# Performance work log

Measured on AMD Instinct MI355X. Metric: run time of the kernel, lower is better.

The kernel has to match this reference:

```python
import jax, jax.numpy as jnp
import numpy as np

# irreps layout: in/out = 32x0e + 8x1o  (dim 32 + 24 = 56), sh = 1x0e + 1x1o (dim 4)
NS, NV = 32, 8
N_NODES, N_EDGES, N_EDGE_FEAT, HIDDEN = 10000, 100000, 64, 64
W_NUMEL = NS*NS + NS*NV + NV*NV + NV*NS  # 1600
EPS = 1e-5
# path normalization (e3nn-style 'component'/'element'):
# fan_in into 0e output = 32 (0x0 path) + 8 (1x1 path) = 40; same for 1o output.
INV40 = 1.0 / np.sqrt(40.0)            # paths with trivial/identity CG net factor
INV120 = 1.0 / np.sqrt(120.0)          # paths with w3j = delta/sqrt(3) extra factor


def setup_inputs() -> dict:
    key = jax.random.key(0)
    ks = jax.random.split(key, 12)
    node_attr = jax.random.normal(ks[0], (N_NODES, 56), dtype=jnp.float32)
    edge_attr = jax.random.normal(ks[1], (N_EDGES, N_EDGE_FEAT), dtype=jnp.float32)
    edge_sh = jax.random.normal(ks[2], (N_EDGES, 4), dtype=jnp.float32)
    edge_index = jax.random.randint(ks[3], (2, N_EDGES), 0, N_NODES, dtype=jnp.int64)
    s1 = 1.0 / np.sqrt(N_EDGE_FEAT)
    s2 = 1.0 / np.sqrt(HIDDEN)
    fc1_w = jax.random.normal(ks[4], (N_EDGE_FEAT, HIDDEN), dtype=jnp.float32) * s1
    fc1_b = jnp.zeros((HIDDEN,), dtype=jnp.float32)
    fc2_w = jax.random.normal(ks[5], (HIDDEN, W_NUMEL), dtype=jnp.float32) * s2
    fc2_b = jnp.zeros((W_NUMEL,), dtype=jnp.float32)
    bn_gamma0 = jnp.ones((NS,), dtype=jnp.float32)
    bn_beta0 = jnp.zeros((NS,), dtype=jnp.float32)
    bn_gamma1 = jnp.ones((NV,), dtype=jnp.float32)
    return dict(node_attr=node_attr, edge_attr=edge_attr, edge_sh=edge_sh,
                edge_index=edge_index, fc1_w=fc1_w, fc1_b=fc1_b,
                fc2_w=fc2_w, fc2_b=fc2_b, bn_gamma0=bn_gamma0,
                bn_beta0=bn_beta0, bn_gamma1=bn_gamma1)


def _forward(node_attr, edge_attr, edge_sh, fc1_w, fc1_b, fc2_w, fc2_b,
             bn_gamma0, bn_beta0, bn_gamma1, edge_index):
    E = edge_attr.shape[0]
    N = node_attr.shape[0]
    edge_src, edge_dst = edge_index[0], edge_index[1]

    # edge MLP -> per-edge tensor-product weights [E, 1600]
    h = jax.nn.relu(edge_attr @ fc1_w + fc1_b)
    w = h @ fc2_w + fc2_b
    o1 = NS * NS            # 0e x 0e -> 0e
    o2 = o1 + NS * NV       # 0e x 1o -> 1o
    o3 = o2 + NV * NV       # 1o x 0e -> 1o
    w00 = w[:, :o1].reshape(E, NS, NS)
    w01 = w[:, o1:o2].reshape(E, NS, NV)
    w10 = w[:, o2:o3].reshape(E, NV, NV)
    w11 = w[:, o3:].reshape(E, NV, NS)

    # gather node features at destination, split into scalar / vector irreps
    x = node_attr[edge_dst]                  # [E, 56]
    x0 = x[:, :NS]                           # [E, 32] scalars
    x1 = x[:, NS:].reshape(E, NV, 3)         # [E, 8, 3] l=1 vectors
    s0 = edge_sh[:, 0]                       # [E]
    s1 = edge_sh[:, 1:4]                     # [E, 3]

    # Clebsch-Gordan paths (w3j(1,1,0)=w3j(1,0,1)=w3j(0,1,1)=delta/sqrt(3))
    out0 = jnp.einsum('eu,euw->ew', x0 * s0[:, None], w00) * INV40 \
         + jnp.einsum('eui,ei,euw->ew', x1, s1, w11) * INV120
    out1 = jnp.einsum('eu,ei,euw->ewi', x0, s1, w01) * INV40 \
         + jnp.einsum('eui,euw->ewi', x1 * s0[:, None, None], w10) * INV40
    tp_out = jnp.concatenate([out0, out1.reshape(E, NV * 3)], axis=-1)  # [E, 56]

    # scatter-mean over edge_src
    sums = jax.ops.segment_sum(tp_out, edge_src, num_segments=N)
    cnt = jax.ops.segment_sum(jnp.ones((E,), tp_out.dtype), edge_src, num_segments=N)
    out = sums / jnp.maximum(cnt, 1.0)[:, None]

    # residual (in_dim == out_dim, pad is a no-op)
    out = out + node_attr

    # e3nn-style BatchNorm (training statistics, reduce='mean')
    sc = out[:, :NS]
    vec = out[:, NS:].reshape(N, NV, 3)
    m = sc.mean(axis=0)
    sc_c = sc - m
    var = (sc_c ** 2).mean(axis=0)
    sc_n = sc_c * jax.lax.rsqrt(var + EPS) * bn_gamma0 + bn_beta0
    vnorm = (vec ** 2).mean(axis=-1).mean(axis=0)          # [NV]
    vec_n = vec * (jax.lax.rsqrt(vnorm + EPS) * bn_gamma1)[None, :, None]
    return jnp.concatenate([sc_n, vec_n.reshape(N, NV * 3)], axis=-1)


def reference(node_attr, edge_attr, edge_sh, edge_index, fc1_w, fc1_b,
              fc2_w, fc2_b, bn_gamma0, bn_beta0, bn_gamma1):
    return _forward(node_attr, edge_attr, edge_sh, fc1_w, fc1_b, fc2_w,
                    fc2_b, bn_gamma0, bn_beta0, bn_gamma1, edge_index)
```

## Files before the change

### kernel.cpp

```cpp
#include <hip/hip_runtime.h>

typedef __attribute__((ext_vector_type(4)))  float f32x4;
typedef __attribute__((ext_vector_type(16))) float f32x16;
typedef __attribute__((ext_vector_type(8)))  short bf16x8;
typedef __attribute__((ext_vector_type(4)))  short short4v;

#define NEDGE 100000
#define NNODE 10000
#define INV40f 0.15811388300841897f
#define INV120f 0.09128709291752769f

__device__ inline short f2bf(float f) {
    unsigned u = __builtin_bit_cast(unsigned, f);
    u = (u + 0x7fffu + ((u >> 16) & 1u)) >> 16;
    return (short)u;
}

__device__ __forceinline__ float bperm(int byteIdx, float v) {
    return __builtin_bit_cast(float,
        __builtin_amdgcn_ds_bpermute(byteIdx, __builtin_bit_cast(int, v)));
}

__device__ __forceinline__ void stage16(const void* gsrc, void* ldst) {
    __builtin_amdgcn_global_load_lds(
        (const __attribute__((address_space(1))) unsigned*)gsrc,
        (__attribute__((address_space(3))) unsigned*)(unsigned long long)(uintptr_t)ldst,
        16, 0, 0);
}

#define MFMA32(A,B,C) __builtin_amdgcn_mfma_f32_32x32x16_bf16((A),(B),(C),0,0,0)

__global__ __launch_bounds__(256) void prep(const float* __restrict__ fc1_w,
                                            const float* __restrict__ fc2_w,
                                            short* __restrict__ fc1_wt,
                                            short* __restrict__ fc2_wt,
                                            float* __restrict__ stats,
                                            int* __restrict__ hist) {
    const int b = blockIdx.x, t = threadIdx.x;
    if (b < 25) {
        __shared__ short tile[64 * 66];
        const int c0 = b * 64;
        #pragma unroll
        for (int rep = 0; rep < 16; rep++) {
            const int idx = rep * 256 + t;
            const int k = idx >> 6, c = idx & 63;
            tile[k * 66 + c] = f2bf(fc2_w[(size_t)k * 1600 + c0 + c]);
        }
        __syncthreads();
        #pragma unroll
        for (int rep = 0; rep < 16; rep++) {
            const int idx = rep * 256 + t;
            const int c = idx >> 6, k = idx & 63;
            fc2_wt[(size_t)(c0 + c) * 64 + k] = tile[k * 66 + c];
        }
    } else if (b == 25) {
        #pragma unroll
        for (int rep = 0; rep < 16; rep++) {
            const int i = rep * 256 + t;
            fc1_wt[(i & 63) * 64 + (i >> 6)] = f2bf(fc1_w[i]);
        }
    } else if (b == 26) {
        if (t < 72) stats[t] = 0.0f;
    } else {
        const int i = (b - 27) * 256 + t;
        if (i < NNODE) hist[i] = 0;
    }
}

__global__ __launch_bounds__(256, 2) void edge_fused(
    const float* __restrict__ node_attr,
    const float* __restrict__ edge_attr,
    const float* __restrict__ edge_sh,
    const int*   __restrict__ edge_index,
    const float* __restrict__ fc1_b,
    const float* __restrict__ fc2_b,
    const short* __restrict__ fc1_wt,
    const short* __restrict__ fc2_wt,
    float* __restrict__ tp_out,
    int*   __restrict__ hist)
{
    __shared__ __align__(16) char lds[41216];
    char* cbA = lds;
    char* cbB = lds + 16384;
    float* bias_s = (float*)(lds + 34816);

    const int tid  = threadIdx.x;
    const int wid  = tid >> 6;
    const int wtid = tid & 63;
    const int l31  = wtid & 31;
    const int half = wtid >> 5;
    const int e0   = blockIdx.x * 128 + wid * 32;
    const bool active = (e0 < NEDGE);

    char*  h_s = cbB + wid * 4096;
    float* shb = (float*)(lds + 32768 + wid * 512);
    const int swzl = (l31 & 7) << 4;

#define STAGE1(CH, BUF, J) do { \
        const int _o = (wid * 4 + (J)) * 1024 + wtid * 16; \
        const int _g = _o ^ (((_o >> 7) & 7) << 4); \
        stage16((const char*)fc2_wt + (CH) * 16384 + _g, (BUF) + (wid * 4 + (J)) * 1024); \
    } while (0)
#define STAGE_FULL(CH, BUF) do { STAGE1(CH,BUF,0); STAGE1(CH,BUF,1); STAGE1(CH,BUF,2); STAGE1(CH,BUF,3); } while (0)

    STAGE_FULL(0, cbA);

    *(f32x4*)(bias_s + tid * 4) = *(const f32x4*)(fc2_b + tid * 4);
    if (tid < 144)
        *(f32x4*)(bias_s + (tid + 256) * 4) = *(const f32x4*)(fc2_b + (tid + 256) * 4);

    int dst_r = 0;
    if (active && wtid < 32) {
        dst_r = edge_index[NEDGE + e0 + wtid];
        atomicAdd(&hist[edge_index[e0 + wtid]], 1);
        *(f32x4*)(shb + wtid * 4) = *(const f32x4*)(edge_sh + (size_t)(e0 + wtid) * 4);
    }

    bf16x8 hb[4];
    f32x4 shv = {0.f, 0.f, 0.f, 0.f};
    float cb1r[16], c10r[12], c11r[4];
    int vs[2];
    vs[0] = l31 * 4;
    vs[1] = (32 + l31) * 4;

    if (active) {
        const int dstm = __shfl(dst_r, l31, 64);
        const float* nap = node_attr + (size_t)dstm * 56;
        shv = *(const f32x4*)(shb + l31 * 4);

        const f32x4 t0 = *(const f32x4*)(nap + half * 16);
        const f32x4 t1 = *(const f32x4*)(nap + half * 16 + 4);
        const f32x4 t2 = *(const f32x4*)(nap + half * 16 + 8);
        const f32x4 t3 = *(const f32x4*)(nap + half * 16 + 12);
        #pragma unroll
        for (int j = 0; j < 4; j++) {
            cb1r[j]      = INV40f * t0[j];
            cb1r[4 + j]  = INV40f * t1[j];
            cb1r[8 + j]  = INV40f * t2[j];
            cb1r[12 + j] = INV40f * t3[j];
        }
        const f32x4 y0 = *(const f32x4*)(nap + 32 + half * 12);
        const f32x4 y1 = *(const f32x4*)(nap + 32 + half * 12 + 4);
        const f32x4 y2 = *(const f32x4*)(nap + 32 + half * 12 + 8);
        float xx[12];
        #pragma unroll
        for (int j = 0; j < 4; j++) { xx[j] = y0[j]; xx[4 + j] = y1[j]; xx[8 + j] = y2[j]; }
        const float i40s0 = INV40f * shv[0];
        #pragma unroll
        for (int k = 0; k < 12; k++) c10r[k] = i40s0 * xx[k];
        #pragma unroll
        for (int e = 0; e < 4; e++)
            c11r[e] = INV120f * (xx[e*3]*shv[1] + xx[e*3+1]*shv[2] + xx[e*3+2]*shv[3]);

        const float* pe = edge_attr + (size_t)(e0 + l31) * 64 + half * 8;
        bf16x8 eb[4];
        #pragma unroll
        for (int s = 0; s < 4; s++) {
            const f32x4 a = *(const f32x4*)(pe + s * 16);
            const f32x4 b = *(const f32x4*)(pe + s * 16 + 4);
            #pragma unroll
            for (int i = 0; i < 4; i++) { eb[s][i] = f2bf(a[i]); eb[s][4 + i] = f2bf(b[i]); }
        }
        #pragma unroll
        for (int g = 0; g < 2; g++) {
            f32x16 c;
            #pragma unroll
            for (int q = 0; q < 4; q++) {
                const f32x4 bq = *(const f32x4*)(fc1_b + g*32 + q*8 + half*4);
                c[q*4+0] = bq[0]; c[q*4+1] = bq[1]; c[q*4+2] = bq[2]; c[q*4+3] = bq[3];
            }
            #pragma unroll
            for (int s = 0; s < 4; s++) {
                const bf16x8 af = *(const bf16x8*)(fc1_wt + (g*32 + l31)*64 + s*16 + half*8);
                c = MFMA32(af, eb[s], c);
            }
            #pragma unroll
            for (int q = 0; q < 4; q++) {
                short4v p;
                #pragma unroll
                for (int j = 0; j < 4; j++) p[j] = f2bf(fmaxf(c[q*4+j], 0.0f));
                *(short4v*)(h_s + (l31*128 + ((g*64 + q*16 + half*8) ^ swzl)));
                *(short4v*)(h_s + (l31*128 + ((g*64 + q*16 + half*8) ^ swzl))) = p;
            }
        }
        #pragma unroll
        for (int s = 0; s < 4; s++)
            hb[s] = *(const bf16x8*)(h_s + (l31*128 + ((s*32 + half*16) ^ swzl)));
    }

    float acc0[16] = {};
    float ab1[4] = {0,0,0,0};
    float b2[12] = {};

    auto mload = [&](const char* cb, int go, int G) -> f32x16 {
        f32x16 c;
        #pragma unroll
        for (int q = 0; q < 4; q++) {
            const f32x4 bq = *(const f32x4*)(bias_s + G*32 + q*8 + half*4);
            c[q*4+0] = bq[0]; c[q*4+1] = bq[1]; c[q*4+2] = bq[2]; c[q*4+3] = bq[3];
        }
        #pragma unroll
        for (int s = 0; s < 4; s++) {
            const bf16x8 a = *(const bf16x8*)(cb + go*4096 + l31*128 + ((s*32 + half*16) ^ swzl));
            c = MFMA32(a, hb[s], c);
        }
        return c;
    };

    auto cons_w00 = [&](const char* cb, int ch) {
        #pragma unroll
        for (int go = 0; go < 4; go++) {
            const int G = ch * 4 + go;
            const f32x16 c = mload(cb, go, G);
            const float cv = shv[0] * bperm(vs[G >> 4], cb1r[G & 15]);
            #pragma unroll
            for (int r = 0; r < 16; r++) acc0[r] += cv * c[r];
        }
    };
    auto cons_w01 = [&](const char* cb, int Gl0) {
        #pragma unroll
        for (int go = 0; go < 4; go++) {
            const int Gl = Gl0 + go;
            const f32x16 c = mload(cb, go, 32 + Gl);
            #pragma unroll
            for (int q = 0; q < 4; q++) {
                const int u = Gl * 4 + q;
                const float cvq = bperm(vs[u >> 4], cb1r[u & 15]);
                #pragma unroll
                for (int j = 0; j < 4; j++) ab1[j] += cvq * c[q*4+j];
            }
        }
    };
    auto cons_w10 = [&](const char* cb) {
        #pragma unroll
        for (int go = 0; go < 2; go++) {
            const f32x16 c = mload(cb, go, 40 + go);
            #pragma unroll
            for (int q = 0; q < 4; q++) {
                const int u = go * 4 + q;
                #pragma unroll
                for (int i = 0; i < 3; i++) {
                    const float cv = bperm(vs[u >> 2], c10r[(u & 3) * 3 + i]);
                    #pragma unroll
                    for (int j = 0; j < 4; j++) b2[j*3+i] += cv * c[q*4+j];
                }
            }
        }
    };
    auto cons_w11_2 = [&](const char* cb, int goBase, int Gl0) {
        #pragma unroll
        for (int go = 0; go < 2; go++) {
            const int Gl = Gl0 + go;
            const f32x16 c = mload(cb, goBase + go, 42 + Gl);
            const float cv = bperm(vs[Gl >> 2], c11r[Gl & 3]);
            #pragma unroll
            for (int r = 0; r < 16; r++) acc0[r] += cv * c[r];
        }
    };
    auto cons_w11_4 = [&](const char* cb, int Gl0) {
        #pragma unroll
        for (int go = 0; go < 4; go++) {
            const int Gl = Gl0 + go;
            const f32x16 c = mload(cb, go, 42 + Gl);
            const float cv = bperm(vs[Gl >> 2], c11r[Gl & 3]);
            #pragma unroll
            for (int r = 0; r < 16; r++) acc0[r] += cv * c[r];
        }
    };

    __syncthreads();
    STAGE_FULL(1,  cbB); if (active) cons_w00(cbA, 0); __syncthreads();
    STAGE_FULL(2,  cbA); if (active) cons_w00(cbB, 1); __syncthreads();
    STAGE_FULL(3,  cbB); if (active) cons_w00(cbA, 2); __syncthreads();
    STAGE_FULL(4,  cbA); if (active) cons_w00(cbB, 3); __syncthreads();
    STAGE_FULL(5,  cbB); if (active) cons_w00(cbA, 4); __syncthreads();
    STAGE_FULL(6,  cbA); if (active) cons_w00(cbB, 5); __syncthreads();
    STAGE_FULL(7,  cbB); if (active) cons_w00(cbA, 6); __syncthreads();
    STAGE_FULL(8,  cbA); if (active) cons_w00(cbB, 7); __syncthreads();
    STAGE_FULL(9,  cbB); if (active) cons_w01(cbA, 0); __syncthreads();
    STAGE_FULL(10, cbA); if (active) cons_w01(cbB, 4); __syncthreads();
    STAGE_FULL(11, cbB); if (active) { cons_w10(cbA); cons_w11_2(cbA, 2, 0); } __syncthreads();
    STAGE_FULL(12, cbA); if (active) cons_w11_4(cbB, 2); __syncthreads();
                         if (active) cons_w11_2(cbA, 0, 6);

    if (!active) return;

    float* orow = tp_out + (size_t)(e0 + l31) * 56;
    #pragma unroll
    for (int q = 0; q < 4; q++)
        *(f32x4*)(orow + q*8 + half*4) = f32x4{acc0[q*4], acc0[q*4+1], acc0[q*4+2], acc0[q*4+3]};
    float ov[12];
    #pragma unroll
    for (int j = 0; j < 4; j++) {
        ov[j*3 + 0] = shv[1] * ab1[j] + b2[j*3 + 0];
        ov[j*3 + 1] = shv[2] * ab1[j] + b2[j*3 + 1];
        ov[j*3 + 2] = shv[3] * ab1[j] + b2[j*3 + 2];
    }
    float* p1 = orow + 32 + half * 12;
    *(f32x4*)(p1)     = f32x4{ov[0], ov[1], ov[2],  ov[3]};
    *(f32x4*)(p1 + 4) = f32x4{ov[4], ov[5], ov[6],  ov[7]};
    *(f32x4*)(p1 + 8) = f32x4{ov[8], ov[9], ov[10], ov[11]};
#undef STAGE1
#undef STAGE_FULL
}

__global__ __launch_bounds__(256) void scan_hist(const int* __restrict__ hist,
                                                 int* __restrict__ offsets,
                                                 int* __restrict__ cursor) {
    __shared__ int wsum[4];
    const int t = threadIdx.x;
    const int lane = t & 63;
    const int w = t >> 6;
    const int n0 = t * 40;
    int s = 0;
    if (n0 < NNODE) {
        for (int j = 0; j < 40; j++) s += hist[n0 + j];
    }
    int incl = s;
    #pragma unroll
    for (int d = 1; d < 64; d <<= 1) {
        const int v = __shfl_up(incl, d, 64);
        if (lane >= d) incl += v;
    }
    if (lane == 63) wsum[w] = incl;
    __syncthreads();
    int base = 0;
    for (int ww = 0; ww < 4; ww++) base += (ww < w) ? wsum[ww] : 0;
    if (n0 < NNODE) {
        int run = base + incl - s;
        for (int j = 0; j < 40; j++) {
            const int h = hist[n0 + j];
            offsets[n0 + j] = run; cursor[n0 + j] = run; run += h;
        }
    }
    if (t == 0) offsets[NNODE] = NEDGE;
}

__global__ __launch_bounds__(256) void fill_perm(const int* __restrict__ edge_index,
                                                 int* __restrict__ cursor,
                                                 int* __restrict__ perm) {
    const int e = blockIdx.x * 256 + threadIdx.x;
    if (e < NEDGE) {
        const int s = edge_index[e];
        const int p = atomicAdd(&cursor[s], 1);
        perm[p] = e;
    }
}

__global__ __launch_bounds__(256) void node_agg(
    const float* __restrict__ tp_out, const int* __restrict__ offsets,
    const int* __restrict__ perm,
    const float* __restrict__ node_attr, float* __restrict__ out,
    float* __restrict__ stats)
{
    __shared__ float part[72];
    const int tid = threadIdx.x;
    if (tid < 72) part[tid] = 0.0f;
    __syncthreads();
    const int n = blockIdx.x * 16 + (tid >> 4);
    const int q = tid & 15;
    if (n < NNODE && q < 14) {
        const int st = offsets[n], en = offsets[n + 1];
        f32x4 acc = {0.f, 0.f, 0.f, 0.f};
        for (int r = st; r < en; r++)
            acc += *(const f32x4*)(tp_out + (size_t)perm[r] * 56 + q * 4);
        const float inv = 1.0f / fmaxf((float)(en - st), 1.0f);
        const int c0 = q * 4;
        const f32x4 res = *(const f32x4*)(node_attr + (size_t)n * 56 + c0);
        f32x4 val;
        #pragma unroll
        for (int j = 0; j < 4; j++) {
            val[j] = acc[j] * inv + res[j];
            const int c = c0 + j;
            if (c < 32) {
                atomicAdd(&part[c], val[j]);
                atomicAdd(&part[32 + c], val[j] * val[j]);
            } else {
                atomicAdd(&part[64 + (c - 32) / 3], val[j] * val[j]);
            }
        }
        *(f32x4*)(out + (size_t)n * 56 + c0) = val;
    }
    __syncthreads();
    if (tid < 72) unsafeAtomicAdd(&stats[tid], part[tid]);
}

__global__ __launch_bounds__(256) void node_norm(
    float* __restrict__ out, const float* __restrict__ stats,
    const float* __restrict__ g0, const float* __restrict__ b0,
    const float* __restrict__ g1)
{
    const int id = blockIdx.x * 256 + threadIdx.x;
    if (id >= NNODE * 56) return;
    const int c = id % 56;
    float val = out[id];
    if (c < 32) {
        const float m   = stats[c]      * (1.0f / NNODE);
        const float ex2 = stats[32 + c] * (1.0f / NNODE);
        const float var = ex2 - m * m;
        val = (val - m) * rsqrtf(var + 1e-5f) * g0[c] + b0[c];
    } else {
        const int v = (c - 32) / 3;
        const float vn = stats[64 + v] * (1.0f / (3.0f * NNODE));
        val = val * rsqrtf(vn + 1e-5f) * g1[v];
    }
    out[id] = val;
}

extern "C" void kernel_launch(void* const* d_in, const int* in_sizes, int n_in,
                              void* d_out, int out_size, void* d_ws, size_t ws_size,
                              hipStream_t stream) {
    const float* node_attr = (const float*)d_in[0];
    const float* edge_attr = (const float*)d_in[1];
    const float* edge_sh   = (const float*)d_in[2];
    const int*   edge_index= (const int*)  d_in[3];
    const float* fc1_w     = (const float*)d_in[4];
    const float* fc1_b     = (const float*)d_in[5];
    const float* fc2_w     = (const float*)d_in[6];
    const float* fc2_b     = (const float*)d_in[7];
    const float* g0        = (const float*)d_in[8];
    const float* b0        = (const float*)d_in[9];
    const float* g1        = (const float*)d_in[10];
    float* out = (float*)d_out;

    char* ws = (char*)d_ws;
    float* stats   = (float*)(ws + 0);
    int*   hist    = (int*)  (ws + 288);
    int*   offsets = (int*)  (ws + 40288);
    int*   cursor  = (int*)  (ws + 80320);
    int*   perm    = (int*)  (ws + 120320);
    short* fc1_wt  = (short*)(ws + 520320);
    short* fc2_wt  = (short*)(ws + 528512);
    float* tp_out  = (float*)(ws + 733312);

    prep<<<67, 256, 0, stream>>>(fc1_w, fc2_w, fc1_wt, fc2_wt, stats, hist);
    edge_fused<<<782, 256, 0, stream>>>(node_attr, edge_attr, edge_sh, edge_index,
                                        fc1_b, fc2_b, fc1_wt, fc2_wt, tp_out, hist);
    scan_hist<<<1, 256, 0, stream>>>(hist, offsets, cursor);
    fill_perm<<<391, 256, 0, stream>>>(edge_index, cursor, perm);
    node_agg<<<625, 256, 0, stream>>>(tp_out, offsets, perm, node_attr, out, stats);
    node_norm<<<2188, 256, 0, stream>>>(out, stats, g0, b0, g1);
}
```

Measured before the change: 105.0 us.

## Triple-buffer fc2 weight staging with explicit vmcnt waits and raw barriers

```diff
diff --git a/kernel.cpp b/kernel.cpp
--- a/kernel.cpp
+++ b/kernel.cpp
@@ -79,10 +79,11 @@
     float* __restrict__ tp_out,
     int*   __restrict__ hist)
 {
-    __shared__ __align__(16) char lds[41216];
-    char* cbA = lds;
-    char* cbB = lds + 16384;
-    float* bias_s = (float*)(lds + 34816);
+    __shared__ __align__(16) char lds[57600];
+    char* bufs0 = lds;
+    char* bufs1 = lds + 16384;
+    char* bufs2 = lds + 32768;
+    float* bias_s = (float*)(lds + 51200);
 
     const int tid  = threadIdx.x;
     const int wid  = tid >> 6;
@@ -92,8 +93,8 @@
     const int e0   = blockIdx.x * 128 + wid * 32;
     const bool active = (e0 < NEDGE);
 
-    char*  h_s = cbB + wid * 4096;
-    float* shb = (float*)(lds + 32768 + wid * 512);
+    char*  h_s = bufs2 + wid * 4096;
+    float* shb = (float*)(lds + 49152 + wid * 512);
     const int swzl = (l31 & 7) << 4;
 
 #define STAGE1(CH, BUF, J) do { \
@@ -103,7 +104,6 @@
     } while (0)
 #define STAGE_FULL(CH, BUF) do { STAGE1(CH,BUF,0); STAGE1(CH,BUF,1); STAGE1(CH,BUF,2); STAGE1(CH,BUF,3); } while (0)
 
-    STAGE_FULL(0, cbA);
 
     *(f32x4*)(bias_s + tid * 4) = *(const f32x4*)(fc2_b + tid * 4);
     if (tid < 144)
@@ -179,7 +179,6 @@
                 short4v p;
                 #pragma unroll
                 for (int j = 0; j < 4; j++) p[j] = f2bf(fmaxf(c[q*4+j], 0.0f));
-                *(short4v*)(h_s + (l31*128 + ((g*64 + q*16 + half*8) ^ swzl)));
                 *(short4v*)(h_s + (l31*128 + ((g*64 + q*16 + half*8) ^ swzl))) = p;
             }
         }
@@ -187,6 +186,15 @@
         for (int s = 0; s < 4; s++)
             hb[s] = *(const bf16x8*)(h_s + (l31*128 + ((s*32 + half*16) ^ swzl)));
     }
+
+    asm volatile("s_waitcnt lgkmcnt(0)" ::: "memory");
+    __builtin_amdgcn_sched_barrier(0);
+    __builtin_amdgcn_s_barrier();
+    __builtin_amdgcn_sched_barrier(0);
+
+    STAGE_FULL(0, bufs0);
+    STAGE_FULL(1, bufs1);
+    STAGE_FULL(2, bufs2);
 
     float acc0[16] = {};
     float ab1[4] = {0,0,0,0};
@@ -268,20 +276,35 @@
         }
     };
 
-    __syncthreads();
-    STAGE_FULL(1,  cbB); if (active) cons_w00(cbA, 0); __syncthreads();
-    STAGE_FULL(2,  cbA); if (active) cons_w00(cbB, 1); __syncthreads();
-    STAGE_FULL(3,  cbB); if (active) cons_w00(cbA, 2); __syncthreads();
-    STAGE_FULL(4,  cbA); if (active) cons_w00(cbB, 3); __syncthreads();
-    STAGE_FULL(5,  cbB); if (active) cons_w00(cbA, 4); __syncthreads();
-    STAGE_FULL(6,  cbA); if (active) cons_w00(cbB, 5); __syncthreads();
-    STAGE_FULL(7,  cbB); if (active) cons_w00(cbA, 6); __syncthreads();
-    STAGE_FULL(8,  cbA); if (active) cons_w00(cbB, 7); __syncthreads();
-    STAGE_FULL(9,  cbB); if (active) cons_w01(cbA, 0); __syncthreads();
-    STAGE_FULL(10, cbA); if (active) cons_w01(cbB, 4); __syncthreads();
-    STAGE_FULL(11, cbB); if (active) { cons_w10(cbA); cons_w11_2(cbA, 2, 0); } __syncthreads();
-    STAGE_FULL(12, cbA); if (active) cons_w11_4(cbB, 2); __syncthreads();
-                         if (active) cons_w11_2(cbA, 0, 6);
+#define WAITBAR(N) do { \
+        asm volatile("s_waitcnt vmcnt(" N ")" ::: "memory"); \
+        __builtin_amdgcn_sched_barrier(0); \
+        __builtin_amdgcn_s_barrier(); \
+        __builtin_amdgcn_sched_barrier(0); \
+    } while (0)
+#define ENDPHASE() do { \
+        __builtin_amdgcn_s_barrier(); \
+        __builtin_amdgcn_sched_barrier(0); \
+    } while (0)
+
+    WAITBAR("8"); if (active) cons_w00(bufs0, 0); ENDPHASE(); STAGE_FULL(3,  bufs0);
+    WAITBAR("8"); if (active) cons_w00(bufs1, 1); ENDPHASE(); STAGE_FULL(4,  bufs1);
+    WAITBAR("8"); if (active) cons_w00(bufs2, 2); ENDPHASE(); STAGE_FULL(5,  bufs2);
+    WAITBAR("8"); if (active) cons_w00(bufs0, 3); ENDPHASE(); STAGE_FULL(6,  bufs0);
+    WAITBAR("8"); if (active) cons_w00(bufs1, 4); ENDPHASE(); STAGE_FULL(7,  bufs1);
+    WAITBAR("8"); if (active) cons_w00(bufs2, 5); ENDPHASE(); STAGE_FULL(8,  bufs2);
+    WAITBAR("8"); if (active) cons_w00(bufs0, 6); ENDPHASE(); STAGE_FULL(9,  bufs0);
+    WAITBAR("8"); if (active) cons_w00(bufs1, 7); ENDPHASE(); STAGE_FULL(10, bufs1);
+    WAITBAR("8"); if (active) cons_w01(bufs2, 0); ENDPHASE(); STAGE_FULL(11, bufs2);
+    WAITBAR("8"); if (active) cons_w01(bufs0, 4); ENDPHASE(); STAGE_FULL(12, bufs0);
+    WAITBAR("8"); if (active) { cons_w10(bufs1); cons_w11_2(bufs1, 2, 0); } ENDPHASE();
+    WAITBAR("4"); if (active) cons_w11_4(bufs2, 2); ENDPHASE();
+    WAITBAR("0"); if (active) cons_w11_2(bufs0, 0, 6);
+
+#undef WAITBAR
+#undef ENDPHASE
+#undef STAGE1
+#undef STAGE_FULL
 
     if (!active) return;
 
@@ -300,8 +323,6 @@
     *(f32x4*)(p1)     = f32x4{ov[0], ov[1], ov[2],  ov[3]};
     *(f32x4*)(p1 + 4) = f32x4{ov[4], ov[5], ov[6],  ov[7]};
     *(f32x4*)(p1 + 8) = f32x4{ov[8], ov[9], ov[10], ov[11]};
-#undef STAGE1
-#undef STAGE_FULL
 }
 
 __global__ __launch_bounds__(256) void scan_hist(const int* __restrict__ hist,
```

Measured after the change: 104.0 us. About the same (-1.0%).

## Pre-permute fc2 weights into MFMA fragment order and widen histogram scan

Applied to the files above, without the earlier changes.

```diff
diff --git a/kernel.cpp b/kernel.cpp
--- a/kernel.cpp
+++ b/kernel.cpp
@@ -47,11 +47,16 @@
             tile[k * 66 + c] = f2bf(fc2_w[(size_t)k * 1600 + c0 + c]);
         }
         __syncthreads();
+        short* outp = fc2_wt + b * 4096;
         #pragma unroll
         for (int rep = 0; rep < 16; rep++) {
-            const int idx = rep * 256 + t;
-            const int c = idx >> 6, k = idx & 63;
-            fc2_wt[(size_t)(c0 + c) * 64 + k] = tile[k * 66 + c];
+            const int og = rep * 256 + t;
+            const int g2rel = og >> 11;
+            const int t2 = (og >> 8) & 7;
+            const int cl = ((og >> 3) & 31) + g2rel * 32;
+            const int j = og & 7;
+            const int k = (t2 >> 1) * 16 + (t2 & 1) * 8 + j;
+            outp[og] = tile[k * 66 + cl];
         }
     } else if (b == 25) {
         #pragma unroll
@@ -98,8 +103,7 @@
 
 #define STAGE1(CH, BUF, J) do { \
         const int _o = (wid * 4 + (J)) * 1024 + wtid * 16; \
-        const int _g = _o ^ (((_o >> 7) & 7) << 4); \
-        stage16((const char*)fc2_wt + (CH) * 16384 + _g, (BUF) + (wid * 4 + (J)) * 1024); \
+        stage16((const char*)fc2_wt + (CH) * 16384 + _o, (BUF) + (wid * 4 + (J)) * 1024); \
     } while (0)
 #define STAGE_FULL(CH, BUF) do { STAGE1(CH,BUF,0); STAGE1(CH,BUF,1); STAGE1(CH,BUF,2); STAGE1(CH,BUF,3); } while (0)
 
@@ -179,7 +183,6 @@
                 short4v p;
                 #pragma unroll
                 for (int j = 0; j < 4; j++) p[j] = f2bf(fmaxf(c[q*4+j], 0.0f));
-                *(short4v*)(h_s + (l31*128 + ((g*64 + q*16 + half*8) ^ swzl)));
                 *(short4v*)(h_s + (l31*128 + ((g*64 + q*16 + half*8) ^ swzl))) = p;
             }
         }
@@ -201,7 +204,7 @@
         }
         #pragma unroll
         for (int s = 0; s < 4; s++) {
-            const bf16x8 a = *(const bf16x8*)(cb + go*4096 + l31*128 + ((s*32 + half*16) ^ swzl));
+            const bf16x8 a = *(const bf16x8*)(cb + go*4096 + (s*2 + half)*512 + l31*16);
             c = MFMA32(a, hb[s], c);
         }
         return c;
@@ -304,33 +307,31 @@
 #undef STAGE_FULL
 }
 
-__global__ __launch_bounds__(256) void scan_hist(const int* __restrict__ hist,
-                                                 int* __restrict__ offsets,
-                                                 int* __restrict__ cursor) {
-    __shared__ int wsum[4];
+__global__ __launch_bounds__(1024) void scan_hist(const int* __restrict__ hist,
+                                                  int* __restrict__ offsets,
+                                                  int* __restrict__ cursor) {
+    __shared__ int part[1024];
     const int t = threadIdx.x;
-    const int lane = t & 63;
-    const int w = t >> 6;
-    const int n0 = t * 40;
+    const int n0 = t * 10;
+    int lh[10];
     int s = 0;
     if (n0 < NNODE) {
-        for (int j = 0; j < 40; j++) s += hist[n0 + j];
-    }
-    int incl = s;
-    #pragma unroll
-    for (int d = 1; d < 64; d <<= 1) {
-        const int v = __shfl_up(incl, d, 64);
-        if (lane >= d) incl += v;
-    }
-    if (lane == 63) wsum[w] = incl;
+        #pragma unroll
+        for (int j = 0; j < 10; j++) { lh[j] = hist[n0 + j]; s += lh[j]; }
+    }
+    part[t] = s;
     __syncthreads();
-    int base = 0;
-    for (int ww = 0; ww < 4; ww++) base += (ww < w) ? wsum[ww] : 0;
+    for (int d = 1; d < 1024; d <<= 1) {
+        const int v = (t >= d) ? part[t - d] : 0;
+        __syncthreads();
+        part[t] += v;
+        __syncthreads();
+    }
     if (n0 < NNODE) {
-        int run = base + incl - s;
-        for (int j = 0; j < 40; j++) {
-            const int h = hist[n0 + j];
-            offsets[n0 + j] = run; cursor[n0 + j] = run; run += h;
+        int run = part[t] - s;
+        #pragma unroll
+        for (int j = 0; j < 10; j++) {
+            offsets[n0 + j] = run; cursor[n0 + j] = run; run += lh[j];
         }
     }
     if (t == 0) offsets[NNODE] = NEDGE;
@@ -436,7 +437,7 @@
     prep<<<67, 256, 0, stream>>>(fc1_w, fc2_w, fc1_wt, fc2_wt, stats, hist);
     edge_fused<<<782, 256, 0, stream>>>(node_attr, edge_attr, edge_sh, edge_index,
                                         fc1_b, fc2_b, fc1_wt, fc2_wt, tp_out, hist);
-    scan_hist<<<1, 256, 0, stream>>>(hist, offsets, cursor);
+    scan_hist<<<1, 1024, 0, stream>>>(hist, offsets, cursor);
     fill_perm<<<391, 256, 0, stream>>>(edge_index, cursor, perm);
     node_agg<<<625, 256, 0, stream>>>(tp_out, offsets, perm, node_attr, out, stats);
     node_norm<<<2188, 256, 0, stream>>>(out, stats, g0, b0, g1);
```

Measured after the change: 101.0 us, median of 2. -3.8%, faster.

## Fuse scan+fill and agg+norm kernels via grid-wide flag spin barriers

Applied to the files above, without the earlier changes.

```diff
diff --git a/kernel.cpp b/kernel.cpp
--- a/kernel.cpp
+++ b/kernel.cpp
@@ -35,7 +35,8 @@
                                             short* __restrict__ fc1_wt,
                                             short* __restrict__ fc2_wt,
                                             float* __restrict__ stats,
-                                            int* __restrict__ hist) {
+                                            int* __restrict__ hist,
+                                            int* __restrict__ flags) {
     const int b = blockIdx.x, t = threadIdx.x;
     if (b < 25) {
         __shared__ short tile[64 * 66];
@@ -47,11 +48,16 @@
             tile[k * 66 + c] = f2bf(fc2_w[(size_t)k * 1600 + c0 + c]);
         }
         __syncthreads();
+        short* outp = fc2_wt + b * 4096;
         #pragma unroll
         for (int rep = 0; rep < 16; rep++) {
-            const int idx = rep * 256 + t;
-            const int c = idx >> 6, k = idx & 63;
-            fc2_wt[(size_t)(c0 + c) * 64 + k] = tile[k * 66 + c];
+            const int og = rep * 256 + t;
+            const int g2rel = og >> 11;
+            const int t2 = (og >> 8) & 7;
+            const int cl = ((og >> 3) & 31) + g2rel * 32;
+            const int j = og & 7;
+            const int k = (t2 >> 1) * 16 + (t2 & 1) * 8 + j;
+            outp[og] = tile[k * 66 + cl];
         }
     } else if (b == 25) {
         #pragma unroll
@@ -61,6 +67,7 @@
         }
     } else if (b == 26) {
         if (t < 72) stats[t] = 0.0f;
+        if (t >= 72 && t < 74) flags[t - 72] = 0;
     } else {
         const int i = (b - 27) * 256 + t;
         if (i < NNODE) hist[i] = 0;
@@ -98,8 +105,7 @@
 
 #define STAGE1(CH, BUF, J) do { \
         const int _o = (wid * 4 + (J)) * 1024 + wtid * 16; \
-        const int _g = _o ^ (((_o >> 7) & 7) << 4); \
-        stage16((const char*)fc2_wt + (CH) * 16384 + _g, (BUF) + (wid * 4 + (J)) * 1024); \
+        stage16((const char*)fc2_wt + (CH) * 16384 + _o, (BUF) + (wid * 4 + (J)) * 1024); \
     } while (0)
 #define STAGE_FULL(CH, BUF) do { STAGE1(CH,BUF,0); STAGE1(CH,BUF,1); STAGE1(CH,BUF,2); STAGE1(CH,BUF,3); } while (0)
 
@@ -179,7 +185,6 @@
                 short4v p;
                 #pragma unroll
                 for (int j = 0; j < 4; j++) p[j] = f2bf(fmaxf(c[q*4+j], 0.0f));
-                *(short4v*)(h_s + (l31*128 + ((g*64 + q*16 + half*8) ^ swzl)));
                 *(short4v*)(h_s + (l31*128 + ((g*64 + q*16 + half*8) ^ swzl))) = p;
             }
         }
@@ -201,7 +206,7 @@
         }
         #pragma unroll
         for (int s = 0; s < 4; s++) {
-            const bf16x8 a = *(const bf16x8*)(cb + go*4096 + l31*128 + ((s*32 + half*16) ^ swzl));
+            const bf16x8 a = *(const bf16x8*)(cb + go*4096 + (s*2 + half)*512 + l31*16);
             c = MFMA32(a, hb[s], c);
         }
         return c;
@@ -304,42 +309,55 @@
 #undef STAGE_FULL
 }
 
-__global__ __launch_bounds__(256) void scan_hist(const int* __restrict__ hist,
-                                                 int* __restrict__ offsets,
-                                                 int* __restrict__ cursor) {
-    __shared__ int wsum[4];
+__global__ __launch_bounds__(256) void scanfill(const int* __restrict__ hist,
+                                                const int* __restrict__ edge_index,
+                                                int* __restrict__ offsets,
+                                                int* __restrict__ cursor,
+                                                int* __restrict__ perm,
+                                                int* __restrict__ flag) {
     const int t = threadIdx.x;
-    const int lane = t & 63;
-    const int w = t >> 6;
-    const int n0 = t * 40;
-    int s = 0;
-    if (n0 < NNODE) {
-        for (int j = 0; j < 40; j++) s += hist[n0 + j];
-    }
-    int incl = s;
-    #pragma unroll
-    for (int d = 1; d < 64; d <<= 1) {
-        const int v = __shfl_up(incl, d, 64);
-        if (lane >= d) incl += v;
-    }
-    if (lane == 63) wsum[w] = incl;
-    __syncthreads();
-    int base = 0;
-    for (int ww = 0; ww < 4; ww++) base += (ww < w) ? wsum[ww] : 0;
-    if (n0 < NNODE) {
-        int run = base + incl - s;
-        for (int j = 0; j < 40; j++) {
-            const int h = hist[n0 + j];
-            offsets[n0 + j] = run; cursor[n0 + j] = run; run += h;
-        }
-    }
-    if (t == 0) offsets[NNODE] = NEDGE;
-}
-
-__global__ __launch_bounds__(256) void fill_perm(const int* __restrict__ edge_index,
-                                                 int* __restrict__ cursor,
-                                                 int* __restrict__ perm) {
-    const int e = blockIdx.x * 256 + threadIdx.x;
+    if (blockIdx.x == 0) {
+        __shared__ int wsum[4];
+        const int lane = t & 63;
+        const int w = t >> 6;
+        const int n0 = t * 40;
+        int s = 0;
+        if (n0 < NNODE) {
+            for (int j = 0; j < 40; j++) s += hist[n0 + j];
+        }
+        int incl = s;
+        #pragma unroll
+        for (int d = 1; d < 64; d <<= 1) {
+            const int v = __shfl_up(incl, d, 64);
+            if (lane >= d) incl += v;
+        }
+        if (lane == 63) wsum[w] = incl;
+        __syncthreads();
+        int base = 0;
+        for (int ww = 0; ww < 4; ww++) base += (ww < w) ? wsum[ww] : 0;
+        if (n0 < NNODE) {
+            int run = base + incl - s;
+            for (int j = 0; j < 40; j++) {
+                const int h = hist[n0 + j];
+                offsets[n0 + j] = run; cursor[n0 + j] = run; run += h;
+            }
+        }
+        if (t == 0) offsets[NNODE] = NEDGE;
+        __syncthreads();
+        if (t == 0) {
+            __threadfence();
+            __hip_atomic_store(flag, 1, __ATOMIC_RELEASE, __HIP_MEMORY_SCOPE_AGENT);
+        }
+        __syncthreads();
+    } else {
+        if (t == 0) {
+            while (__hip_atomic_load(flag, __ATOMIC_ACQUIRE, __HIP_MEMORY_SCOPE_AGENT) == 0)
+                __builtin_amdgcn_s_sleep(2);
+        }
+        __syncthreads();
+        __threadfence();
+    }
+    const int e = blockIdx.x * 256 + t;
     if (e < NEDGE) {
         const int s = edge_index[e];
         const int p = atomicAdd(&cursor[s], 1);
@@ -347,11 +365,13 @@
     }
 }
 
-__global__ __launch_bounds__(256) void node_agg(
+__global__ __launch_bounds__(256) void node_aggnorm(
     const float* __restrict__ tp_out, const int* __restrict__ offsets,
     const int* __restrict__ perm,
     const float* __restrict__ node_attr, float* __restrict__ out,
-    float* __restrict__ stats)
+    float* __restrict__ stats, int* __restrict__ done,
+    const float* __restrict__ g0, const float* __restrict__ b0,
+    const float* __restrict__ g1)
 {
     __shared__ float part[72];
     const int tid = threadIdx.x;
@@ -359,15 +379,16 @@
     __syncthreads();
     const int n = blockIdx.x * 16 + (tid >> 4);
     const int q = tid & 15;
-    if (n < NNODE && q < 14) {
+    const bool act = (q < 14);
+    f32x4 val = {0.f, 0.f, 0.f, 0.f};
+    const int c0 = q * 4;
+    if (act) {
         const int st = offsets[n], en = offsets[n + 1];
         f32x4 acc = {0.f, 0.f, 0.f, 0.f};
         for (int r = st; r < en; r++)
-            acc += *(const f32x4*)(tp_out + (size_t)perm[r] * 56 + q * 4);
+            acc += *(const f32x4*)(tp_out + (size_t)perm[r] * 56 + c0);
         const float inv = 1.0f / fmaxf((float)(en - st), 1.0f);
-        const int c0 = q * 4;
         const f32x4 res = *(const f32x4*)(node_attr + (size_t)n * 56 + c0);
-        f32x4 val;
         #pragma unroll
         for (int j = 0; j < 4; j++) {
             val[j] = acc[j] * inv + res[j];
@@ -379,32 +400,35 @@
                 atomicAdd(&part[64 + (c - 32) / 3], val[j] * val[j]);
             }
         }
-        *(f32x4*)(out + (size_t)n * 56 + c0) = val;
     }
     __syncthreads();
     if (tid < 72) unsafeAtomicAdd(&stats[tid], part[tid]);
-}
-
-__global__ __launch_bounds__(256) void node_norm(
-    float* __restrict__ out, const float* __restrict__ stats,
-    const float* __restrict__ g0, const float* __restrict__ b0,
-    const float* __restrict__ g1)
-{
-    const int id = blockIdx.x * 256 + threadIdx.x;
-    if (id >= NNODE * 56) return;
-    const int c = id % 56;
-    float val = out[id];
-    if (c < 32) {
-        const float m   = stats[c]      * (1.0f / NNODE);
-        const float ex2 = stats[32 + c] * (1.0f / NNODE);
-        const float var = ex2 - m * m;
-        val = (val - m) * rsqrtf(var + 1e-5f) * g0[c] + b0[c];
-    } else {
-        const int v = (c - 32) / 3;
-        const float vn = stats[64 + v] * (1.0f / (3.0f * NNODE));
-        val = val * rsqrtf(vn + 1e-5f) * g1[v];
-    }
-    out[id] = val;
+    __syncthreads();
+    if (tid == 0) {
+        __threadfence();
+        atomicAdd(done, 1);
+        while (__hip_atomic_load(done, __ATOMIC_ACQUIRE, __HIP_MEMORY_SCOPE_AGENT) < 625)
+            __builtin_amdgcn_s_sleep(2);
+    }
+    __syncthreads();
+    __threadfence();
+    if (act) {
+        #pragma unroll
+        for (int j = 0; j < 4; j++) {
+            const int c = c0 + j;
+            if (c < 32) {
+                const float m   = stats[c]      * (1.0f / NNODE);
+                const float ex2 = stats[32 + c] * (1.0f / NNODE);
+                const float var = ex2 - m * m;
+                val[j] = (val[j] - m) * rsqrtf(var + 1e-5f) * g0[c] + b0[c];
+            } else {
+                const int v = (c - 32) / 3;
+                const float vn = stats[64 + v] * (1.0f / (3.0f * NNODE));
+                val[j] = val[j] * rsqrtf(vn + 1e-5f) * g1[v];
+            }
+        }
+        *(f32x4*)(out + (size_t)n * 56 + c0) = val;
+    }
 }
 
 extern "C" void kernel_launch(void* const* d_in, const int* in_sizes, int n_in,
@@ -427,17 +451,17 @@
     float* stats   = (float*)(ws + 0);
     int*   hist    = (int*)  (ws + 288);
     int*   offsets = (int*)  (ws + 40288);
+    int*   flags   = (int*)  (ws + 80296);
     int*   cursor  = (int*)  (ws + 80320);
     int*   perm    = (int*)  (ws + 120320);
     short* fc1_wt  = (short*)(ws + 520320);
     short* fc2_wt  = (short*)(ws + 528512);
     float* tp_out  = (float*)(ws + 733312);
 
-    prep<<<67, 256, 0, stream>>>(fc1_w, fc2_w, fc1_wt, fc2_wt, stats, hist);
+    prep<<<67, 256, 0, stream>>>(fc1_w, fc2_w, fc1_wt, fc2_wt, stats, hist, flags);
     edge_fused<<<782, 256, 0, stream>>>(node_attr, edge_attr, edge_sh, edge_index,
                                         fc1_b, fc2_b, fc1_wt, fc2_wt, tp_out, hist);
-    scan_hist<<<1, 256, 0, stream>>>(hist, offsets, cursor);
-    fill_perm<<<391, 256, 0, stream>>>(edge_index, cursor, perm);
-    node_agg<<<625, 256, 0, stream>>>(tp_out, offsets, perm, node_attr, out, stats);
-    node_norm<<<2188, 256, 0, stream>>>(out, stats, g0, b0, g1);
-}
+    scanfill<<<391, 256, 0, stream>>>(hist, edge_index, offsets, cursor, perm, flags);
+    node_aggnorm<<<625, 256, 0, stream>>>(tp_out, offsets, perm, node_attr, out,
+                                          stats, flags + 1, g0, b0, g1);
+}
```

Result: slower. 324.2 us (+208.8%).
